# Optimization experiments

Measured on AMD Instinct MI355X. Metric: run time of the kernel, lower is better.

The kernel has to match this reference:

```python
import math
import jax, jax.numpy as jnp
import numpy as np

N_HEAD = 16

def setup_inputs() -> dict:
    key = jax.random.key(0)
    k1, k2, k3 = jax.random.split(key, 3)
    B, T, C = 4, 2048, 1024
    x = jax.random.normal(k1, (B, T, C), dtype=jnp.float32)
    Wqkv = jax.random.normal(k2, (C, 3 * C), dtype=jnp.float32) * (1.0 / math.sqrt(C))
    bqkv = jnp.zeros((3 * C,), dtype=jnp.float32)
    Wproj = jax.random.normal(k3, (C, C), dtype=jnp.float32) * (1.0 / math.sqrt(C))
    bproj = jnp.zeros((C,), dtype=jnp.float32)
    return {"x": x, "Wqkv": Wqkv, "bqkv": bqkv, "Wproj": Wproj, "bproj": bproj}

def reference(x, Wqkv, bqkv, Wproj, bproj):
    B, T, C = x.shape
    H = N_HEAD
    D = C // H
    # fused QKV projection
    qkv = x @ Wqkv + bqkv                      # [B,T,3C]
    qkv = qkv.reshape(B, T, 3, H, D).transpose(0, 2, 3, 1, 4)  # [B,3,H,T,D]
    q, k, v = qkv[:, 0], qkv[:, 1], qkv[:, 2]  # each [B,H,T,D]
    scale = 1.0 / math.sqrt(D)
    att = jnp.einsum('bhtd,bhsd->bhts', q, k) * scale  # [B,H,T,T]
    # causal mask: disallow s > t
    mask = jnp.triu(jnp.ones((T, T), dtype=bool), k=1)
    att = jnp.where(mask, jnp.float32(-1e9), att)
    att = jax.nn.softmax(att, axis=-1)
    y = jnp.einsum('bhts,bhsd->bhtd', att, v)  # [B,H,T,D]
    y = y.transpose(0, 2, 1, 3).reshape(B, T, C)
    y = y @ Wproj + bproj
    return y
```

## Files before the change

kernel.cpp:

```cpp
#include <hip/hip_runtime.h>
#include <hip/hip_bf16.h>

#define B_ 4
#define T_ 2048
#define C_ 1024
#define H_ 16
#define D_ 64

typedef __attribute__((ext_vector_type(8))) short short8;
typedef __attribute__((ext_vector_type(4))) float f32x4;

#define QSCALE 0.18033688011112042f

static __device__ __forceinline__ unsigned short f2bf(float f) {
  unsigned u = __float_as_uint(f);
  u += 0x7fff + ((u >> 16) & 1);
  return (unsigned short)(u >> 16);
}

static __device__ __forceinline__ float fast_exp2(float x) {
#if __has_builtin(__builtin_amdgcn_exp2f)
  return __builtin_amdgcn_exp2f(x);
#else
  return exp2f(x);
#endif
}

#define GL2LDS16(g, l)                                              \
  __builtin_amdgcn_global_load_lds(                                 \
      (const __attribute__((address_space(1))) void*)(g),           \
      (__attribute__((address_space(3))) void*)(l), 16, 0, 0)

__global__ __launch_bounds__(256) void prepass(
    const float* __restrict__ x, const float* __restrict__ Wq,
    const float* __restrict__ Wp, ushort* __restrict__ xb,
    ushort* __restrict__ Wqt, ushort* __restrict__ Wpt) {
  __shared__ ushort tile[32][33];
  const int bid = blockIdx.x;
  if (bid < 8192) {
    const size_t i = ((size_t)bid * 256 + threadIdx.x) * 4;
    float4 vv = *(const float4*)(x + i);
    ushort4 o = {f2bf(vv.x), f2bf(vv.y), f2bf(vv.z), f2bf(vv.w)};
    *(ushort4*)(xb + i) = o;
    return;
  }
  const float* in;
  ushort* out;
  int N, tix;
  if (bid < 8192 + 3072) {
    in = Wq; out = Wqt; N = 3 * C_; tix = bid - 8192;
  } else {
    in = Wp; out = Wpt; N = C_; tix = bid - 11264;
  }
  const int nT = N >> 5;
  const int k0 = (tix / nT) << 5, n0 = (tix % nT) << 5;
  const int r = threadIdx.x >> 3;
  const int c4 = (threadIdx.x & 7) << 2;
  float4 v = *(const float4*)(in + (size_t)(k0 + r) * N + n0 + c4);
  tile[c4 + 0][r] = f2bf(v.x);
  tile[c4 + 1][r] = f2bf(v.y);
  tile[c4 + 2][r] = f2bf(v.z);
  tile[c4 + 3][r] = f2bf(v.w);
  __syncthreads();
  ushort4 o = {tile[r][c4], tile[r][c4 + 1], tile[r][c4 + 2], tile[r][c4 + 3]};
  *(ushort4*)(out + (size_t)(n0 + r) * C_ + k0 + c4) = o;
}

static __device__ __forceinline__ void swz_src(int wave, int lane, int p,
                                               int& row, int& off) {
  const int f = p * 256 + wave * 64 + lane;
  const int P = f >> 3, pos = f & 7;
  const int x = pos ^ (P & 7);
  row = 2 * P + (x >> 2);
  off = (x & 3) * 8;
}
static __device__ __forceinline__ int swz_frag(int r, int quad) {
  const int P = r >> 1;
  const int pos = (((r & 1) << 2) | quad) ^ (P & 7);
  return (P * 8 + pos) * 16;
}

__global__ __launch_bounds__(256) void gemm_qkv_mfma(
    const ushort* __restrict__ A, const ushort* __restrict__ Bt,
    const float* __restrict__ bias, ushort* __restrict__ q,
    ushort* __restrict__ k, ushort* __restrict__ v) {
  __shared__ __align__(16) ushort As[128 * 32];
  __shared__ __align__(16) ushort Bs[128 * 32];
  const int tid = threadIdx.x;
  const int wave = tid >> 6, lane = tid & 63;
  const int c = lane & 15, quad = lane >> 4;
  const int wm = wave & 1, wn = wave >> 1;
  const int m0 = blockIdx.y << 7;
  const int n0 = blockIdx.x << 7;

  int srcRow[2], srcOff[2];
#pragma unroll
  for (int p = 0; p < 2; ++p) swz_src(wave, lane, p, srcRow[p], srcOff[p]);
  int fOffA[4], fOffB[4];
#pragma unroll
  for (int i = 0; i < 4; ++i) fOffA[i] = swz_frag(wm * 64 + i * 16 + c, quad);
#pragma unroll
  for (int j = 0; j < 4; ++j) fOffB[j] = swz_frag(wn * 64 + j * 16 + c, quad);

  f32x4 acc[4][4];
#pragma unroll
  for (int i = 0; i < 4; ++i)
#pragma unroll
    for (int j = 0; j < 4; ++j) acc[i][j] = (f32x4){0.f, 0.f, 0.f, 0.f};

  for (int k0 = 0; k0 < C_; k0 += 32) {
    __syncthreads();
#pragma unroll
    for (int p = 0; p < 2; ++p) {
      GL2LDS16(A + (size_t)(m0 + srcRow[p]) * C_ + k0 + srcOff[p],
               (char*)As + p * 4096 + wave * 1024);
      GL2LDS16(Bt + (size_t)(n0 + srcRow[p]) * C_ + k0 + srcOff[p],
               (char*)Bs + p * 4096 + wave * 1024);
    }
    __syncthreads();

    short8 af[4], bf[4];
#pragma unroll
    for (int i = 0; i < 4; ++i)
      af[i] = *(const short8*)((const char*)As + fOffA[i]);
#pragma unroll
    for (int j = 0; j < 4; ++j)
      bf[j] = *(const short8*)((const char*)Bs + fOffB[j]);
#pragma unroll
    for (int i = 0; i < 4; ++i)
#pragma unroll
      for (int j = 0; j < 4; ++j)
        acc[i][j] =
            __builtin_amdgcn_mfma_f32_16x16x32_bf16(af[i], bf[j], acc[i][j], 0, 0, 0);
  }

  const int s = n0 >> 10;
  if (s == 2) {
#pragma unroll
    for (int j = 0; j < 4; ++j) {
      const int n = n0 + wn * 64 + j * 16 + c;
      const int h = (n >> 6) & 15, d = n & 63;
      const float bval = bias[n];
#pragma unroll
      for (int i = 0; i < 4; ++i) {
        const int m = m0 + wm * 64 + i * 16 + quad * 4;
        const int b = m >> 11, t = m & 2047;
        ushort4 pk = {f2bf(acc[i][j][0] + bval), f2bf(acc[i][j][1] + bval),
                      f2bf(acc[i][j][2] + bval), f2bf(acc[i][j][3] + bval)};
        *(ushort4*)(v + (((size_t)((b << 4) + h) << 6) + d) * T_ + t) = pk;
      }
    }
  } else {
    ushort* outp = (s == 0) ? q : k;
    const float sc = (s == 0) ? QSCALE : 1.0f;
#pragma unroll
    for (int j = 0; j < 4; ++j) {
      const int n = n0 + wn * 64 + j * 16 + c;
      const int h = (n >> 6) & 15, d = n & 63;
      const float bval = bias[n];
#pragma unroll
      for (int i = 0; i < 4; ++i) {
#pragma unroll
        for (int r = 0; r < 4; ++r) {
          const int m = m0 + wm * 64 + i * 16 + quad * 4 + r;
          const int b = m >> 11, t = m & 2047;
          outp[(((size_t)((b << 4) + h) << 11) + t) * 64 + d] =
              f2bf((acc[i][j][r] + bval) * sc);
        }
      }
    }
  }
}

__global__ __launch_bounds__(256) void gemm_proj_mfma(
    const ushort* __restrict__ A, const ushort* __restrict__ Bt,
    const float* __restrict__ bias, float* __restrict__ out) {
  __shared__ __align__(16) ushort As[128 * 32];
  __shared__ __align__(16) ushort Bs[128 * 32];
  const int tid = threadIdx.x;
  const int wave = tid >> 6, lane = tid & 63;
  const int c = lane & 15, quad = lane >> 4;
  const int wm = wave & 1, wn = wave >> 1;
  const int m0 = blockIdx.y << 7;
  const int n0 = blockIdx.x << 7;

  int srcRow[2], srcOff[2];
#pragma unroll
  for (int p = 0; p < 2; ++p) swz_src(wave, lane, p, srcRow[p], srcOff[p]);
  int fOffA[4], fOffB[4];
#pragma unroll
  for (int i = 0; i < 4; ++i) fOffA[i] = swz_frag(wm * 64 + i * 16 + c, quad);
#pragma unroll
  for (int j = 0; j < 4; ++j) fOffB[j] = swz_frag(wn * 64 + j * 16 + c, quad);

  f32x4 acc[4][4];
#pragma unroll
  for (int i = 0; i < 4; ++i)
#pragma unroll
    for (int j = 0; j < 4; ++j) acc[i][j] = (f32x4){0.f, 0.f, 0.f, 0.f};

  for (int k0 = 0; k0 < C_; k0 += 32) {
    __syncthreads();
#pragma unroll
    for (int p = 0; p < 2; ++p) {
      GL2LDS16(A + (size_t)(m0 + srcRow[p]) * C_ + k0 + srcOff[p],
               (char*)As + p * 4096 + wave * 1024);
      GL2LDS16(Bt + (size_t)(n0 + srcRow[p]) * C_ + k0 + srcOff[p],
               (char*)Bs + p * 4096 + wave * 1024);
    }
    __syncthreads();

    short8 af[4], bf[4];
#pragma unroll
    for (int i = 0; i < 4; ++i)
      af[i] = *(const short8*)((const char*)As + fOffA[i]);
#pragma unroll
    for (int j = 0; j < 4; ++j)
      bf[j] = *(const short8*)((const char*)Bs + fOffB[j]);
#pragma unroll
    for (int i = 0; i < 4; ++i)
#pragma unroll
      for (int j = 0; j < 4; ++j)
        acc[i][j] =
            __builtin_amdgcn_mfma_f32_16x16x32_bf16(af[i], bf[j], acc[i][j], 0, 0, 0);
  }

#pragma unroll
  for (int j = 0; j < 4; ++j) {
    const int n = n0 + wn * 64 + j * 16 + c;
    const float bval = bias[n];
#pragma unroll
    for (int i = 0; i < 4; ++i) {
#pragma unroll
      for (int r = 0; r < 4; ++r) {
        const int m = m0 + wm * 64 + i * 16 + quad * 4 + r;
        out[(size_t)m * C_ + n] = acc[i][j][r] + bval;
      }
    }
  }
}

__global__ __launch_bounds__(256) void attn(const ushort* __restrict__ q,
                                            const ushort* __restrict__ k,
                                            const ushort* __restrict__ v,
                                            ushort* __restrict__ y2) {
  const int qt = 15 - (int)(blockIdx.x >> 6);
  const int bh = blockIdx.x & 63;
  const int t0 = qt << 7;
  const int w = threadIdx.x >> 6;
  const int lane = threadIdx.x & 63;
  const int c = lane & 15;
  const int quad = lane >> 4;

  const ushort* qp = q + (size_t)bh * T_ * D_;
  const ushort* kp = k + (size_t)bh * T_ * D_;
  const ushort* vp = v + (size_t)bh * D_ * T_;

  __shared__ __align__(16) ushort Ks[64][72];
  __shared__ __align__(16) ushort Vs[64][72];
  __shared__ __align__(16) ushort Ps[4][32][72];

  short8 qf[2][2];
#pragma unroll
  for (int g = 0; g < 2; ++g) {
    const ushort* qrow = qp + (size_t)(t0 + 32 * w + 16 * g + c) * D_;
    qf[g][0] = *(const short8*)(qrow + quad * 8);
    qf[g][1] = *(const short8*)(qrow + 32 + quad * 8);
  }

  const int srow = threadIdx.x >> 2;
  const int soff = (threadIdx.x & 3) << 4;

  uint4 ka, kb, va, vb;
  {
    const ushort* ks = kp + (size_t)srow * D_ + soff;
    const ushort* vs = vp + (size_t)srow * T_ + soff;
    ka = *(const uint4*)(ks);
    kb = *(const uint4*)(ks + 8);
    va = *(const uint4*)(vs);
    vb = *(const uint4*)(vs + 8);
  }

  f32x4 o[2][4];
  float l_i[2] = {0.f, 0.f};
#pragma unroll
  for (int g = 0; g < 2; ++g)
#pragma unroll
    for (int dt = 0; dt < 4; ++dt) o[g][dt] = (f32x4){0.f, 0.f, 0.f, 0.f};

  const int nb = 2 * qt + 2;
  for (int ib = 0; ib < nb; ++ib) {
    const int s0 = ib << 6;
    __syncthreads();
    *(uint4*)(&Ks[srow][soff]) = ka;
    *(uint4*)(&Ks[srow][soff + 8]) = kb;
    *(uint4*)(&Vs[srow][soff]) = va;
    *(uint4*)(&Vs[srow][soff + 8]) = vb;
    __syncthreads();

    if (ib + 1 < nb) {
      const int s1 = (ib + 1) << 6;
      const ushort* ks = kp + (size_t)(s1 + srow) * D_ + soff;
      const ushort* vs = vp + (size_t)srow * T_ + s1 + soff;
      ka = *(const uint4*)(ks);
      kb = *(const uint4*)(ks + 8);
      va = *(const uint4*)(vs);
      vb = *(const uint4*)(vs + 8);
    }

#pragma unroll
    for (int g = 0; g < 2; ++g) {
      f32x4 st[4];
#pragma unroll
      for (int kt = 0; kt < 4; ++kt) {
        short8 af0 = *(const short8*)(&Ks[kt * 16 + c][quad * 8]);
        short8 af1 = *(const short8*)(&Ks[kt * 16 + c][32 + quad * 8]);
        f32x4 a = (f32x4){0.f, 0.f, 0.f, 0.f};
        a = __builtin_amdgcn_mfma_f32_16x16x32_bf16(af0, qf[g][0], a, 0, 0, 0);
        a = __builtin_amdgcn_mfma_f32_16x16x32_bf16(af1, qf[g][1], a, 0, 0, 0);
        st[kt] = a;
      }

      const int qbase = t0 + 32 * w + 16 * g;
      if (s0 + 63 > qbase) {
#pragma unroll
        for (int kt = 0; kt < 4; ++kt)
#pragma unroll
          for (int r = 0; r < 4; ++r)
            if (s0 + kt * 16 + 4 * quad + r > qbase + c) st[kt][r] = -1e30f;
      }

      float lacc = 0.f;
#pragma unroll
      for (int kt = 0; kt < 4; ++kt) {
        float p0 = fast_exp2(st[kt][0]);
        float p1 = fast_exp2(st[kt][1]);
        float p2 = fast_exp2(st[kt][2]);
        float p3 = fast_exp2(st[kt][3]);
        lacc += (p0 + p1) + (p2 + p3);
        ushort4 pk = {f2bf(p0), f2bf(p1), f2bf(p2), f2bf(p3)};
        *(ushort4*)(&Ps[w][g * 16 + c][kt * 16 + 4 * quad]) = pk;
      }
      l_i[g] += lacc;
    }

    short8 pf[2][2];
#pragma unroll
    for (int g = 0; g < 2; ++g) {
      pf[g][0] = *(const short8*)(&Ps[w][g * 16 + c][quad * 8]);
      pf[g][1] = *(const short8*)(&Ps[w][g * 16 + c][32 + quad * 8]);
    }
#pragma unroll
    for (int dt = 0; dt < 4; ++dt) {
      short8 vf0 = *(const short8*)(&Vs[dt * 16 + c][quad * 8]);
      short8 vf1 = *(const short8*)(&Vs[dt * 16 + c][32 + quad * 8]);
#pragma unroll
      for (int g = 0; g < 2; ++g) {
        o[g][dt] =
            __builtin_amdgcn_mfma_f32_16x16x32_bf16(vf0, pf[g][0], o[g][dt], 0, 0, 0);
        o[g][dt] =
            __builtin_amdgcn_mfma_f32_16x16x32_bf16(vf1, pf[g][1], o[g][dt], 0, 0, 0);
      }
    }
  }

  float linv[2];
#pragma unroll
  for (int g = 0; g < 2; ++g) {
    float ls = l_i[g];
    ls += __shfl_xor(ls, 16);
    ls += __shfl_xor(ls, 32);
    linv[g] = 1.0f / ls;
  }

  const int b = bh >> 4, h = bh & 15;
#pragma unroll
  for (int g = 0; g < 2; ++g) {
    const int row = t0 + 32 * w + 16 * g + c;
    ushort* dst = y2 + (size_t)(b * T_ + row) * C_ + h * 64;
#pragma unroll
    for (int dt = 0; dt < 4; ++dt) {
      ushort4 ov = {f2bf(o[g][dt][0] * linv[g]), f2bf(o[g][dt][1] * linv[g]),
                    f2bf(o[g][dt][2] * linv[g]), f2bf(o[g][dt][3] * linv[g])};
      *(ushort4*)(dst + dt * 16 + 4 * quad) = ov;
    }
  }
}

extern "C" void kernel_launch(void* const* d_in, const int* in_sizes, int n_in,
                              void* d_out, int out_size, void* d_ws,
                              size_t ws_size, hipStream_t stream) {
  const float* x = (const float*)d_in[0];
  const float* Wqkv = (const float*)d_in[1];
  const float* bqkv = (const float*)d_in[2];
  const float* Wproj = (const float*)d_in[3];
  const float* bproj = (const float*)d_in[4];
  float* out = (float*)d_out;

  const size_t per = (size_t)B_ * H_ * T_ * D_;
  ushort* q = (ushort*)d_ws;
  ushort* k = q + per;
  ushort* v = k + per;
  ushort* y2 = v + per;
  ushort* xb = y2 + per;
  ushort* Wqkvt = xb + per;
  ushort* Wprojt = Wqkvt + 3 * C_ * C_;

  prepass<<<dim3(12288), 256, 0, stream>>>(x, Wqkv, Wproj, xb, Wqkvt, Wprojt);
  gemm_qkv_mfma<<<dim3(24, 64), 256, 0, stream>>>(xb, Wqkvt, bqkv, q, k, v);
  attn<<<dim3(1024), 256, 0, stream>>>(q, k, v, y2);
  gemm_proj_mfma<<<dim3(8, 64), 256, 0, stream>>>(y2, Wprojt, bproj, out);
}
```

Baseline: 261.7 us.

## Remap GEMM block order, transpose MFMA operands for vectorized stores, reorder attention QK loop

The QKV GEMM now uses a 1D grid with a remapped tile order that interleaves N tiles across the Q/K/V sections. Both GEMMs swap MFMA operand order so each lane holds four consecutive output columns, which allows 8-byte bf16 stores for Q/K, float4 stores for the projection output, and vector bias loads in place of scattered scalar writes. In attention, the QK^T loop is reordered so each K fragment is loaded from LDS once and used for both query groups. The costs are more live score registers and a duplicated main loop in the QKV GEMM.

```diff
diff --git a/kernel.cpp b/kernel.cpp
--- a/kernel.cpp
+++ b/kernel.cpp
@@ -86,12 +86,15 @@
     ushort* __restrict__ k, ushort* __restrict__ v) {
   __shared__ __align__(16) ushort As[128 * 32];
   __shared__ __align__(16) ushort Bs[128 * 32];
+  const int id = blockIdx.x;
+  const int nt = (id & 7) * 3 + ((id >> 3) % 3);
+  const int mt = id / 24;
+  const int m0 = mt << 7;
+  const int n0 = nt << 7;
   const int tid = threadIdx.x;
   const int wave = tid >> 6, lane = tid & 63;
   const int c = lane & 15, quad = lane >> 4;
   const int wm = wave & 1, wn = wave >> 1;
-  const int m0 = blockIdx.y << 7;
-  const int n0 = blockIdx.x << 7;
 
   int srcRow[2], srcOff[2];
 #pragma unroll
@@ -108,34 +111,33 @@
 #pragma unroll
     for (int j = 0; j < 4; ++j) acc[i][j] = (f32x4){0.f, 0.f, 0.f, 0.f};
 
-  for (int k0 = 0; k0 < C_; k0 += 32) {
-    __syncthreads();
-#pragma unroll
-    for (int p = 0; p < 2; ++p) {
-      GL2LDS16(A + (size_t)(m0 + srcRow[p]) * C_ + k0 + srcOff[p],
-               (char*)As + p * 4096 + wave * 1024);
-      GL2LDS16(Bt + (size_t)(n0 + srcRow[p]) * C_ + k0 + srcOff[p],
-               (char*)Bs + p * 4096 + wave * 1024);
-    }
-    __syncthreads();
-
-    short8 af[4], bf[4];
-#pragma unroll
-    for (int i = 0; i < 4; ++i)
-      af[i] = *(const short8*)((const char*)As + fOffA[i]);
-#pragma unroll
-    for (int j = 0; j < 4; ++j)
-      bf[j] = *(const short8*)((const char*)Bs + fOffB[j]);
-#pragma unroll
-    for (int i = 0; i < 4; ++i)
+  const int s = n0 >> 10;
+
+  if (s == 2) {
+    for (int k0 = 0; k0 < C_; k0 += 32) {
+      __syncthreads();
+#pragma unroll
+      for (int p = 0; p < 2; ++p) {
+        GL2LDS16(A + (size_t)(m0 + srcRow[p]) * C_ + k0 + srcOff[p],
+                 (char*)As + p * 4096 + wave * 1024);
+        GL2LDS16(Bt + (size_t)(n0 + srcRow[p]) * C_ + k0 + srcOff[p],
+                 (char*)Bs + p * 4096 + wave * 1024);
+      }
+      __syncthreads();
+      short8 af[4], bf[4];
+#pragma unroll
+      for (int i = 0; i < 4; ++i)
+        af[i] = *(const short8*)((const char*)As + fOffA[i]);
 #pragma unroll
       for (int j = 0; j < 4; ++j)
-        acc[i][j] =
-            __builtin_amdgcn_mfma_f32_16x16x32_bf16(af[i], bf[j], acc[i][j], 0, 0, 0);
-  }
-
-  const int s = n0 >> 10;
-  if (s == 2) {
+        bf[j] = *(const short8*)((const char*)Bs + fOffB[j]);
+#pragma unroll
+      for (int i = 0; i < 4; ++i)
+#pragma unroll
+        for (int j = 0; j < 4; ++j)
+          acc[i][j] = __builtin_amdgcn_mfma_f32_16x16x32_bf16(af[i], bf[j],
+                                                              acc[i][j], 0, 0, 0);
+    }
 #pragma unroll
     for (int j = 0; j < 4; ++j) {
       const int n = n0 + wn * 64 + j * 16 + c;
@@ -151,22 +153,46 @@
       }
     }
   } else {
+    for (int k0 = 0; k0 < C_; k0 += 32) {
+      __syncthreads();
+#pragma unroll
+      for (int p = 0; p < 2; ++p) {
+        GL2LDS16(A + (size_t)(m0 + srcRow[p]) * C_ + k0 + srcOff[p],
+                 (char*)As + p * 4096 + wave * 1024);
+        GL2LDS16(Bt + (size_t)(n0 + srcRow[p]) * C_ + k0 + srcOff[p],
+                 (char*)Bs + p * 4096 + wave * 1024);
+      }
+      __syncthreads();
+      short8 af[4], bf[4];
+#pragma unroll
+      for (int i = 0; i < 4; ++i)
+        af[i] = *(const short8*)((const char*)As + fOffA[i]);
+#pragma unroll
+      for (int j = 0; j < 4; ++j)
+        bf[j] = *(const short8*)((const char*)Bs + fOffB[j]);
+#pragma unroll
+      for (int i = 0; i < 4; ++i)
+#pragma unroll
+        for (int j = 0; j < 4; ++j)
+          acc[j][i] = __builtin_amdgcn_mfma_f32_16x16x32_bf16(bf[j], af[i],
+                                                              acc[j][i], 0, 0, 0);
+    }
     ushort* outp = (s == 0) ? q : k;
     const float sc = (s == 0) ? QSCALE : 1.0f;
 #pragma unroll
     for (int j = 0; j < 4; ++j) {
-      const int n = n0 + wn * 64 + j * 16 + c;
-      const int h = (n >> 6) & 15, d = n & 63;
-      const float bval = bias[n];
+      const int nb4 = n0 + wn * 64 + j * 16 + quad * 4;
+      const int h = (nb4 >> 6) & 15, d0 = nb4 & 63;
+      float4 b4 = *(const float4*)(bias + nb4);
 #pragma unroll
       for (int i = 0; i < 4; ++i) {
-#pragma unroll
-        for (int r = 0; r < 4; ++r) {
-          const int m = m0 + wm * 64 + i * 16 + quad * 4 + r;
-          const int b = m >> 11, t = m & 2047;
-          outp[(((size_t)((b << 4) + h) << 11) + t) * 64 + d] =
-              f2bf((acc[i][j][r] + bval) * sc);
-        }
+        const int m = m0 + wm * 64 + i * 16 + c;
+        const int b = m >> 11, t = m & 2047;
+        ushort4 pk = {f2bf((acc[j][i][0] + b4.x) * sc),
+                      f2bf((acc[j][i][1] + b4.y) * sc),
+                      f2bf((acc[j][i][2] + b4.z) * sc),
+                      f2bf((acc[j][i][3] + b4.w) * sc)};
+        *(ushort4*)(outp + (((size_t)((b << 4) + h) << 11) + t) * 64 + d0) = pk;
       }
     }
   }
@@ -177,12 +203,13 @@
     const float* __restrict__ bias, float* __restrict__ out) {
   __shared__ __align__(16) ushort As[128 * 32];
   __shared__ __align__(16) ushort Bs[128 * 32];
+  const int id = blockIdx.x;
+  const int m0 = (id >> 3) << 7;
+  const int n0 = (id & 7) << 7;
   const int tid = threadIdx.x;
   const int wave = tid >> 6, lane = tid & 63;
   const int c = lane & 15, quad = lane >> 4;
   const int wm = wave & 1, wn = wave >> 1;
-  const int m0 = blockIdx.y << 7;
-  const int n0 = blockIdx.x << 7;
 
   int srcRow[2], srcOff[2];
 #pragma unroll
@@ -209,7 +236,6 @@
                (char*)Bs + p * 4096 + wave * 1024);
     }
     __syncthreads();
-
     short8 af[4], bf[4];
 #pragma unroll
     for (int i = 0; i < 4; ++i)
@@ -221,21 +247,20 @@
     for (int i = 0; i < 4; ++i)
 #pragma unroll
       for (int j = 0; j < 4; ++j)
-        acc[i][j] =
-            __builtin_amdgcn_mfma_f32_16x16x32_bf16(af[i], bf[j], acc[i][j], 0, 0, 0);
+        acc[j][i] = __builtin_amdgcn_mfma_f32_16x16x32_bf16(bf[j], af[i],
+                                                            acc[j][i], 0, 0, 0);
   }
 
 #pragma unroll
   for (int j = 0; j < 4; ++j) {
-    const int n = n0 + wn * 64 + j * 16 + c;
-    const float bval = bias[n];
+    const int nb4 = n0 + wn * 64 + j * 16 + quad * 4;
+    float4 b4 = *(const float4*)(bias + nb4);
 #pragma unroll
     for (int i = 0; i < 4; ++i) {
-#pragma unroll
-      for (int r = 0; r < 4; ++r) {
-        const int m = m0 + wm * 64 + i * 16 + quad * 4 + r;
-        out[(size_t)m * C_ + n] = acc[i][j][r] + bval;
-      }
+      const int m = m0 + wm * 64 + i * 16 + c;
+      float4 ov = {acc[j][i][0] + b4.x, acc[j][i][1] + b4.y,
+                   acc[j][i][2] + b4.z, acc[j][i][3] + b4.w};
+      *(float4*)(out + (size_t)m * C_ + nb4) = ov;
     }
   }
 }
@@ -308,35 +333,37 @@
       vb = *(const uint4*)(vs + 8);
     }
 
-#pragma unroll
-    for (int g = 0; g < 2; ++g) {
-      f32x4 st[4];
-#pragma unroll
-      for (int kt = 0; kt < 4; ++kt) {
-        short8 af0 = *(const short8*)(&Ks[kt * 16 + c][quad * 8]);
-        short8 af1 = *(const short8*)(&Ks[kt * 16 + c][32 + quad * 8]);
+    f32x4 st[2][4];
+#pragma unroll
+    for (int kt = 0; kt < 4; ++kt) {
+      short8 af0 = *(const short8*)(&Ks[kt * 16 + c][quad * 8]);
+      short8 af1 = *(const short8*)(&Ks[kt * 16 + c][32 + quad * 8]);
+#pragma unroll
+      for (int g = 0; g < 2; ++g) {
         f32x4 a = (f32x4){0.f, 0.f, 0.f, 0.f};
         a = __builtin_amdgcn_mfma_f32_16x16x32_bf16(af0, qf[g][0], a, 0, 0, 0);
         a = __builtin_amdgcn_mfma_f32_16x16x32_bf16(af1, qf[g][1], a, 0, 0, 0);
-        st[kt] = a;
-      }
-
+        st[g][kt] = a;
+      }
+    }
+
+#pragma unroll
+    for (int g = 0; g < 2; ++g) {
       const int qbase = t0 + 32 * w + 16 * g;
       if (s0 + 63 > qbase) {
 #pragma unroll
         for (int kt = 0; kt < 4; ++kt)
 #pragma unroll
           for (int r = 0; r < 4; ++r)
-            if (s0 + kt * 16 + 4 * quad + r > qbase + c) st[kt][r] = -1e30f;
-      }
-
+            if (s0 + kt * 16 + 4 * quad + r > qbase + c) st[g][kt][r] = -1e30f;
+      }
       float lacc = 0.f;
 #pragma unroll
       for (int kt = 0; kt < 4; ++kt) {
-        float p0 = fast_exp2(st[kt][0]);
-        float p1 = fast_exp2(st[kt][1]);
-        float p2 = fast_exp2(st[kt][2]);
-        float p3 = fast_exp2(st[kt][3]);
+        float p0 = fast_exp2(st[g][kt][0]);
+        float p1 = fast_exp2(st[g][kt][1]);
+        float p2 = fast_exp2(st[g][kt][2]);
+        float p3 = fast_exp2(st[g][kt][3]);
         lacc += (p0 + p1) + (p2 + p3);
         ushort4 pk = {f2bf(p0), f2bf(p1), f2bf(p2), f2bf(p3)};
         *(ushort4*)(&Ps[w][g * 16 + c][kt * 16 + 4 * quad]) = pk;
@@ -407,7 +434,7 @@
   ushort* Wprojt = Wqkvt + 3 * C_ * C_;
 
   prepass<<<dim3(12288), 256, 0, stream>>>(x, Wqkv, Wproj, xb, Wqkvt, Wprojt);
-  gemm_qkv_mfma<<<dim3(24, 64), 256, 0, stream>>>(xb, Wqkvt, bqkv, q, k, v);
+  gemm_qkv_mfma<<<dim3(1536), 256, 0, stream>>>(xb, Wqkvt, bqkv, q, k, v);
   attn<<<dim3(1024), 256, 0, stream>>>(q, k, v, y2);
-  gemm_proj_mfma<<<dim3(8, 64), 256, 0, stream>>>(y2, Wprojt, bproj, out);
-}
+  gemm_proj_mfma<<<dim3(512), 256, 0, stream>>>(y2, Wprojt, bproj, out);
+}
```

Result: slower. 268.8 us (+2.7%).
